# Kernel tuning notes

Measured on AMD Instinct MI355X. Metric: run time of the kernel, lower is better.

Reference implementation:

```python
import jax, jax.numpy as jnp
import numpy as np
import math

N_NODES = 100000
N_EDGES = 500000
HEADS = 8
IN_CH = 128          # dim(x) + dim(feats) = 64 + 64
OUT_CH = 128         # heads * 16
HEAD_DIM = OUT_CH // HEADS
MSG_DIM = 64
TIME_DIM = 64
EDGE_DIM = MSG_DIM + TIME_DIM


def setup_inputs() -> dict:
    key = jax.random.key(0)
    ks = jax.random.split(key, 16)
    p = lambda k, shp: (jax.random.normal(k, shp, dtype=jnp.float32) * 0.02)
    return {
        "feats": jax.random.normal(ks[0], (N_NODES, 64), dtype=jnp.float32),
        "x": jax.random.normal(ks[1], (N_NODES, 64), dtype=jnp.float32),
        "last_update": jax.random.uniform(ks[2], (N_NODES,), dtype=jnp.float32),
        "edge_index": jax.random.randint(ks[3], (2, N_EDGES), 0, N_NODES, dtype=jnp.int64),
        "t": jax.random.uniform(ks[4], (N_EDGES,), dtype=jnp.float32),
        "msg": jax.random.normal(ks[5], (N_EDGES, MSG_DIM), dtype=jnp.float32),
        # TimeEncoder: cos(Linear(1, TIME_DIM)(t))
        "time_w": p(ks[6], (TIME_DIM,)),
        "time_b": p(ks[7], (TIME_DIM,)),
        # TransformerConv params
        "Wq": p(ks[8], (IN_CH, OUT_CH)),
        "bq": jnp.zeros((OUT_CH,), jnp.float32),
        "Wk": p(ks[9], (IN_CH, OUT_CH)),
        "bk": jnp.zeros((OUT_CH,), jnp.float32),
        "Wv": p(ks[10], (IN_CH, OUT_CH)),
        "bv": jnp.zeros((OUT_CH,), jnp.float32),
        "We": p(ks[11], (EDGE_DIM, OUT_CH)),   # lin_edge, bias=False in PyG
        "Wskip": p(ks[12], (IN_CH, OUT_CH)),   # root weight skip connection
        "bskip": jnp.zeros((OUT_CH,), jnp.float32),
    }


def reference(feats, x, last_update, edge_index, t, msg,
              time_w, time_b, Wq, bq, Wk, bk, Wv, bv, We, Wskip, bskip):
    N = feats.shape[0]
    src, dst = edge_index[0], edge_index[1]  # message flows src -> dst

    # relative time encoding (TGN time encoder: cos(w*t + b))
    rel_t = last_update[src] - t                                  # [E]
    rel_t_enc = jnp.cos(rel_t[:, None] * time_w[None, :] + time_b)  # [E, TIME_DIM]
    edge_attr = jnp.concatenate([rel_t_enc, msg], axis=-1)        # [E, EDGE_DIM]

    h = jnp.concatenate([x, feats], axis=-1)                      # [N, IN_CH]

    q = (h @ Wq + bq).reshape(N, HEADS, HEAD_DIM)
    k = (h @ Wk + bk).reshape(N, HEADS, HEAD_DIM)
    v = (h @ Wv + bv).reshape(N, HEADS, HEAD_DIM)
    e = (edge_attr @ We).reshape(-1, HEADS, HEAD_DIM)             # [E, H, C]

    k_e = k[src] + e                                              # [E, H, C]
    alpha = jnp.sum(q[dst] * k_e, axis=-1) / math.sqrt(HEAD_DIM)  # [E, H]

    # segment softmax over incoming edges of each dst node
    m = jax.ops.segment_max(alpha, dst, num_segments=N)           # [N, H]
    m = jnp.where(jnp.isfinite(m), m, 0.0)
    ex = jnp.exp(alpha - m[dst])
    s = jax.ops.segment_sum(ex, dst, num_segments=N)              # [N, H]
    a = ex / (s[dst] + 1e-16)                                     # [E, H]

    out_e = (v[src] + e) * a[..., None]                           # [E, H, C]
    out = jax.ops.segment_sum(out_e, dst, num_segments=N)         # [N, H, C]
    out = out.reshape(N, HEADS * HEAD_DIM)
    return out + h @ Wskip + bskip
```

## Files before the change

kernel.cpp:

```cpp
#include <hip/hip_runtime.h>
#include <math.h>


typedef __attribute__((ext_vector_type(8))) short bf16x8;
typedef __attribute__((ext_vector_type(4))) float f32x4;

__device__ inline short f2bf(float f) {
  unsigned u = __float_as_uint(f);
  u += 0x7fff + ((u >> 16) & 1);
  return (short)(u >> 16);
}
__device__ inline float bf2f(short s) {
  return __uint_as_float(((unsigned)(unsigned short)s) << 16);
}
__device__ inline float bflo(unsigned u) { return __uint_as_float(u << 16); }
__device__ inline float bfhi(unsigned u) { return __uint_as_float(u & 0xffff0000u); }

__global__ void k_hist(const int* __restrict__ ei, int* __restrict__ counts, int E) {
  int i = blockIdx.x * 256 + threadIdx.x;
  if (i < E) atomicAdd(&counts[ei[E + i]], 1);
}

__global__ __launch_bounds__(1024) void k_bsum(const int* __restrict__ counts,
                                               int* __restrict__ bsum, int N) {
  int i = blockIdx.x * 1024 + threadIdx.x;
  int v = (i < N) ? counts[i] : 0;
  for (int d = 32; d; d >>= 1) v += __shfl_down(v, d);
  __shared__ int ws_[16];
  int lane = threadIdx.x & 63, wv = threadIdx.x >> 6;
  if (lane == 0) ws_[wv] = v;
  __syncthreads();
  if (threadIdx.x == 0) {
    int s = 0;
    for (int j = 0; j < 16; ++j) s += ws_[j];
    bsum[blockIdx.x] = s;
  }
}

__global__ __launch_bounds__(128) void k_bscan(const int* __restrict__ bsum,
                                               int* __restrict__ bpre, int nb) {
  __shared__ int sh[128];
  int t = threadIdx.x;
  sh[t] = (t < nb) ? bsum[t] : 0;
  __syncthreads();
  for (int d = 1; d < 128; d <<= 1) {
    int v = (t >= d) ? sh[t - d] : 0;
    __syncthreads();
    sh[t] += v;
    __syncthreads();
  }
  if (t < nb) bpre[t] = (t == 0) ? 0 : sh[t - 1];
}

__global__ __launch_bounds__(1024) void k_scan2(const int* __restrict__ counts,
                                                const int* __restrict__ bpre,
                                                int* __restrict__ offs,
                                                int* __restrict__ cursor, int N) {
  __shared__ int sh[1024];
  int t = threadIdx.x;
  int i = blockIdx.x * 1024 + t;
  int v = (i < N) ? counts[i] : 0;
  sh[t] = v;
  __syncthreads();
  for (int d = 1; d < 1024; d <<= 1) {
    int u = (t >= d) ? sh[t - d] : 0;
    __syncthreads();
    sh[t] += u;
    __syncthreads();
  }
  if (i < N) {
    int excl = bpre[blockIdx.x] + sh[t] - v;
    offs[i] = excl;
    cursor[i] = excl;
    if (i == N - 1) offs[N] = excl + v;
  }
}

__global__ void k_scatter(const int* __restrict__ ei, int* __restrict__ cursor,
                          int* __restrict__ rank, int* __restrict__ src_s, int E) {
  int i = blockIdx.x * 256 + threadIdx.x;
  if (i < E) {
    int pos = atomicAdd(&cursor[ei[E + i]], 1);
    rank[i] = pos;
    src_s[pos] = ei[i];
  }
}

struct PrepArgs { const float* W[5]; };
__global__ void k_prep(PrepArgs pa, short* __restrict__ wf) {
  int tid = blockIdx.x * 256 + threadIdx.x;
  if (tid >= 5 * 8 * 4 * 64) return;
  int lane = tid & 63;
  int kt = (tid >> 6) & 3;
  int nt = (tid >> 8) & 7;
  int mat = tid >> 11;
  const float* W = pa.W[mat];
  int n = nt * 16 + (lane & 15);
  short v[8];
#pragma unroll
  for (int j = 0; j < 8; ++j) {
    int k = kt * 32 + ((j >> 2) * 16) + ((lane >> 4) * 4) + (j & 3);
    v[j] = f2bf(W[k * 128 + n]);
  }
  ((uint4*)wf)[tid] = *(uint4*)v;
}

struct NodeArgs {
  const short* wf;
  const float* bias[4];
  void* outp[4];
};

__global__ __launch_bounds__(256, 2) void k_node(
    const float* __restrict__ x, const float* __restrict__ feats,
    NodeArgs na, int N) {
  __shared__ char lds[4][8192];
  const int lane = threadIdx.x & 63;
  const int wv = threadIdx.x >> 6;
  char* myl = lds[wv];

  bf16x8 bfrag[8][4];
  const uint4* wfp = (const uint4*)na.wf + (size_t)wv * 2048;
#pragma unroll
  for (int nt = 0; nt < 8; ++nt)
#pragma unroll
    for (int kt = 0; kt < 4; ++kt)
      *(uint4*)&bfrag[nt][kt] = wfp[(nt * 4 + kt) * 64 + lane];

  float biasv[8];
#pragma unroll
  for (int nt = 0; nt < 8; ++nt) biasv[nt] = na.bias[wv][nt * 16 + (lane & 15)];
  void* op = na.outp[wv];

  const int arow = lane & 15;
  const int k4 = (lane >> 4) * 4;
  const int ntiles = (N + 15) / 16;
  for (int tile = blockIdx.x; tile < ntiles; tile += gridDim.x) {
    int row = tile * 16 + arow;
    bool valid = row < N;
    const float* xr = x + (size_t)row * 64;
    const float* fr = feats + (size_t)row * 64;
    bf16x8 afrag[4];
#pragma unroll
    for (int kt = 0; kt < 4; ++kt) {
      const float* src = (kt < 2) ? xr : fr;
      int base = (kt & 1) * 32 + k4;
      float4 lo = valid ? *(const float4*)(src + base) : make_float4(0, 0, 0, 0);
      float4 hi = valid ? *(const float4*)(src + base + 16) : make_float4(0, 0, 0, 0);
      bf16x8 a;
      a[0] = f2bf(lo.x); a[1] = f2bf(lo.y); a[2] = f2bf(lo.z); a[3] = f2bf(lo.w);
      a[4] = f2bf(hi.x); a[5] = f2bf(hi.y); a[6] = f2bf(hi.z); a[7] = f2bf(hi.w);
      afrag[kt] = a;
    }
#pragma unroll
    for (int nt = 0; nt < 8; ++nt) {
      f32x4 acc = {0.f, 0.f, 0.f, 0.f};
#pragma unroll
      for (int kt = 0; kt < 4; ++kt)
        acc = __builtin_amdgcn_mfma_f32_16x16x32_bf16(afrag[kt], bfrag[nt][kt], acc, 0, 0, 0);
      int col = nt * 16 + (lane & 15);
#pragma unroll
      for (int reg = 0; reg < 4; ++reg) {
        int r = (lane >> 4) * 4 + reg;
        float vv = acc[reg] + biasv[nt];
        if (wv < 3) ((short*)myl)[r * 128 + col] = f2bf(vv);
        else        ((float*)myl)[r * 128 + col] = vv;
      }
    }
    if (wv < 3) {
      short* opp = (short*)op;
#pragma unroll
      for (int i = 0; i < 8; ++i) {
        int r = i * 2 + (lane >> 5);
        int orow = tile * 16 + r;
        uint2 val = ((const uint2*)myl)[i * 64 + lane];
        if (orow < N)
          *(uint2*)(opp + (size_t)orow * 128 + (lane & 31) * 4) = val;
      }
    } else {
      float* opp = (float*)op;
#pragma unroll
      for (int i = 0; i < 8; ++i) {
        int r = i * 2 + (lane >> 5);
        int orow = tile * 16 + r;
        uint4 val = ((const uint4*)myl)[i * 64 + lane];
        if (orow < N)
          *(uint4*)(opp + (size_t)orow * 128 + (lane & 31) * 4) = val;
      }
    }
  }
}

__global__ __launch_bounds__(512) void k_egemm(
    const float* __restrict__ lu, const int* __restrict__ ei,
    const float* __restrict__ t, const float* __restrict__ msg,
    const float* __restrict__ tw, const float* __restrict__ tb,
    const short* __restrict__ wf, const int* __restrict__ rank,
    short* __restrict__ e_s, int E) {
  __shared__ uint4 wlds[2048];
  __shared__ char tbuf[8][4096];
  const int lane = threadIdx.x & 63;
  const int wv = threadIdx.x >> 6;
  char* myl = tbuf[wv];

  for (int i = threadIdx.x; i < 2048; i += 512)
    wlds[i] = ((const uint4*)wf)[8192 + i];
  __syncthreads();

  const int k4 = (lane >> 4) * 4;
  float twv[16], tbv[16];
#pragma unroll
  for (int kt = 0; kt < 2; ++kt) {
    int base = kt * 32 + k4;
    *(float4*)&twv[kt * 8]     = *(const float4*)(tw + base);
    *(float4*)&twv[kt * 8 + 4] = *(const float4*)(tw + base + 16);
    *(float4*)&tbv[kt * 8]     = *(const float4*)(tb + base);
    *(float4*)&tbv[kt * 8 + 4] = *(const float4*)(tb + base + 16);
  }

  const int ntiles = (E + 15) / 16;
  const int nwaves = gridDim.x * 8;
  for (int tile = blockIdx.x * 8 + wv; tile < ntiles; tile += nwaves) {
    const int e0 = tile * 16;
    int rank16 = 0;
    float relt = 0.f;
    if (lane < 16 && e0 + lane < E) {
      int src = ei[e0 + lane];
      relt = lu[src] - t[e0 + lane];
      rank16 = rank[e0 + lane];
    }
    const int r = lane & 15;
    float my_relt = __shfl(relt, r);
    bool rvalid = (e0 + r) < E;

    bf16x8 afrag[4];
#pragma unroll
    for (int kt = 0; kt < 2; ++kt) {
      bf16x8 a;
#pragma unroll
      for (int j = 0; j < 8; ++j)
        a[j] = f2bf(__cosf(my_relt * twv[kt * 8 + j] + tbv[kt * 8 + j]));
      afrag[kt] = a;
    }
    const float* mr = msg + (size_t)(e0 + r) * 64;
#pragma unroll
    for (int kt = 2; kt < 4; ++kt) {
      int base = (kt - 2) * 32 + k4;
      float4 lo = rvalid ? *(const float4*)(mr + base) : make_float4(0, 0, 0, 0);
      float4 hi = rvalid ? *(const float4*)(mr + base + 16) : make_float4(0, 0, 0, 0);
      bf16x8 a;
      a[0] = f2bf(lo.x); a[1] = f2bf(lo.y); a[2] = f2bf(lo.z); a[3] = f2bf(lo.w);
      a[4] = f2bf(hi.x); a[5] = f2bf(hi.y); a[6] = f2bf(hi.z); a[7] = f2bf(hi.w);
      afrag[kt] = a;
    }

#pragma unroll
    for (int nt = 0; nt < 8; ++nt) {
      bf16x8 bfrag[4];
#pragma unroll
      for (int kt = 0; kt < 4; ++kt)
        *(uint4*)&bfrag[kt] = wlds[(nt * 4 + kt) * 64 + lane];
      f32x4 acc = {0.f, 0.f, 0.f, 0.f};
#pragma unroll
      for (int kt = 0; kt < 4; ++kt)
        acc = __builtin_amdgcn_mfma_f32_16x16x32_bf16(afrag[kt], bfrag[kt], acc, 0, 0, 0);
      int col = nt * 16 + (lane & 15);
#pragma unroll
      for (int reg = 0; reg < 4; ++reg) {
        int rr = (lane >> 4) * 4 + reg;
        ((short*)myl)[rr * 128 + col] = f2bf(acc[reg]);
      }
    }
#pragma unroll
    for (int i = 0; i < 8; ++i) {
      int rr = i * 2 + (lane >> 5);
      int er = e0 + rr;
      int drow = __shfl(rank16, rr);
      uint2 val = ((const uint2*)myl)[i * 64 + lane];
      if (er < E)
        *(uint2*)(e_s + (size_t)drow * 128 + (lane & 31) * 4) = val;
    }
  }
}

__global__ __launch_bounds__(256) void k_agg(
    const int* __restrict__ offs, const int* __restrict__ src_s,
    const short* __restrict__ e_s, const short* __restrict__ qb,
    const short* __restrict__ kb, const short* __restrict__ vb,
    float* __restrict__ out, int N) {
  __shared__ int lds_vo[4][64];
  const int wave = threadIdx.x >> 6;
  const int lane = threadIdx.x & 63;
  const int n = blockIdx.x * 4 + wave;
  if (n >= N) return;
  const int c2 = lane * 2;

  const int off = offs[n], end = offs[n + 1];
  unsigned qv = *(const unsigned*)(qb + (size_t)n * 128 + c2);
  float2 o = *(float2*)(out + (size_t)n * 128 + c2);
  if (end == off) return;
  const float q0 = bflo(qv), q1 = bfhi(qv);

  float s = 0.f, acc0 = 0.f, acc1 = 0.f;

  for (int c0 = off; c0 < end; c0 += 64) {
    const int cnt = min(64, end - c0);
    if (lane < cnt) lds_vo[wave][lane] = src_s[c0 + lane] * 128;
    const int lim = cnt - 1;
    for (int g0 = 0; g0 < cnt; g0 += 8) {
      unsigned evr[8], kvr[8], vvr[8];
#pragma unroll
      for (int g = 0; g < 8; ++g) {
        int jj = g0 + g;
        jj = (jj > lim) ? lim : jj;
        int vo = lds_vo[wave][jj];
        evr[g] = *(const unsigned*)(e_s + (size_t)(c0 + jj) * 128 + c2);
        kvr[g] = *(const unsigned*)(kb + vo + c2);
        vvr[g] = *(const unsigned*)(vb + vo + c2);
      }
#pragma unroll
      for (int g = 0; g < 8; ++g) {
        float part = q0 * (bflo(kvr[g]) + bflo(evr[g]))
                   + q1 * (bfhi(kvr[g]) + bfhi(evr[g]));
        part += __shfl_xor(part, 1);
        part += __shfl_xor(part, 2);
        part += __shfl_xor(part, 4);
        float p = (g0 + g <= lim) ? __expf(part * 0.25f) : 0.f;
        s += p;
        acc0 = fmaf(p, bflo(vvr[g]) + bflo(evr[g]), acc0);
        acc1 = fmaf(p, bfhi(vvr[g]) + bfhi(evr[g]), acc1);
      }
    }
  }
  float r = 1.f / (s + 1e-16f);
  o.x += acc0 * r;
  o.y += acc1 * r;
  *(float2*)(out + (size_t)n * 128 + c2) = o;
}

extern "C" void kernel_launch(void* const* d_in, const int* in_sizes, int n_in,
                              void* d_out, int out_size, void* d_ws, size_t ws_size,
                              hipStream_t stream) {
  const float* feats = (const float*)d_in[0];
  const float* x     = (const float*)d_in[1];
  const float* lu    = (const float*)d_in[2];
  const int*   ei    = (const int*)d_in[3];
  const float* t     = (const float*)d_in[4];
  const float* msg   = (const float*)d_in[5];
  const float* tw    = (const float*)d_in[6];
  const float* tb    = (const float*)d_in[7];
  const float* Wq    = (const float*)d_in[8];
  const float* bq    = (const float*)d_in[9];
  const float* Wk    = (const float*)d_in[10];
  const float* bk    = (const float*)d_in[11];
  const float* Wv    = (const float*)d_in[12];
  const float* bv    = (const float*)d_in[13];
  const float* We    = (const float*)d_in[14];
  const float* Wskip = (const float*)d_in[15];
  const float* bskip = (const float*)d_in[16];
  float* out = (float*)d_out;
  const int N = in_sizes[2];
  const int E = in_sizes[4];

  char* ws = (char*)d_ws;
  short* wfrag = (short*)ws; ws += 5 * 2048 * 16;
  short* qb    = (short*)ws; ws += (size_t)N * 128 * 2;
  short* kbuf  = (short*)ws; ws += (size_t)N * 128 * 2;
  short* vbuf  = (short*)ws; ws += (size_t)N * 128 * 2;
  short* e_s   = (short*)ws; ws += (size_t)E * 128 * 2;
  int* counts  = (int*)ws;   ws += (size_t)(N + 1) * 4;
  int* offs    = (int*)ws;   ws += (size_t)(N + 1) * 4;
  int* cursor  = (int*)ws;   ws += (size_t)N * 4;
  int* rank    = (int*)ws;   ws += (size_t)E * 4;
  int* src_s   = (int*)ws;   ws += (size_t)E * 4;
  int* bsum    = (int*)ws;   ws += 128 * 4;
  int* bpre    = (int*)ws;   ws += 128 * 4;

  const int nb = (N + 1023) / 1024;

  hipMemsetAsync(counts, 0, (size_t)(N + 1) * 4, stream);
  k_hist<<<(E + 255) / 256, 256, 0, stream>>>(ei, counts, E);
  k_bsum<<<nb, 1024, 0, stream>>>(counts, bsum, N);
  k_bscan<<<1, 128, 0, stream>>>(bsum, bpre, nb);
  k_scan2<<<nb, 1024, 0, stream>>>(counts, bpre, offs, cursor, N);
  k_scatter<<<(E + 255) / 256, 256, 0, stream>>>(ei, cursor, rank, src_s, E);

  PrepArgs pa;
  pa.W[0] = Wq; pa.W[1] = Wk; pa.W[2] = Wv; pa.W[3] = Wskip; pa.W[4] = We;
  k_prep<<<40, 256, 0, stream>>>(pa, wfrag);

  NodeArgs na;
  na.wf = wfrag;
  na.bias[0] = bq; na.bias[1] = bk; na.bias[2] = bv; na.bias[3] = bskip;
  na.outp[0] = qb; na.outp[1] = kbuf; na.outp[2] = vbuf; na.outp[3] = out;
  k_node<<<768, 256, 0, stream>>>(x, feats, na, N);

  k_egemm<<<512, 512, 0, stream>>>(lu, ei, t, msg, tw, tb, wfrag,
                                   rank, e_s, E);
  k_agg<<<(N + 3) / 4, 256, 0, stream>>>(offs, src_s, e_s, qb, kbuf, vbuf,
                                         out, N);
}
```

Before: 278.7 us.

## Process two nodes per wave in aggregation and swizzle LDS staging buffers

The aggregation kernel now assigns each half-wave to a separate destination node, with every lane handling four channels through 8-byte loads. This halves the number of idle lanes at low-degree nodes and cuts the shuffle reduction from three steps to two. Separately, the LDS staging buffers in the node and edge GEMMs use an XOR swizzle to reduce bank conflicts when writing the MFMA output. The cost is more registers per lane and less parallelism across channels for high-degree nodes.

```diff
diff --git a/kernel.cpp b/kernel.cpp
--- a/kernel.cpp
+++ b/kernel.cpp
@@ -163,8 +163,13 @@
       for (int reg = 0; reg < 4; ++reg) {
         int r = (lane >> 4) * 4 + reg;
         float vv = acc[reg] + biasv[nt];
-        if (wv < 3) ((short*)myl)[r * 128 + col] = f2bf(vv);
-        else        ((float*)myl)[r * 128 + col] = vv;
+        if (wv < 3) {
+          int wb = (r * 256 + col * 2) ^ (((r >> 2) & 3) << 5);
+          *(short*)(myl + wb) = f2bf(vv);
+        } else {
+          int wb = (r * 512 + col * 4) ^ (((r >> 2) & 3) << 6);
+          *(float*)(myl + wb) = vv;
+        }
       }
     }
     if (wv < 3) {
@@ -173,7 +178,8 @@
       for (int i = 0; i < 8; ++i) {
         int r = i * 2 + (lane >> 5);
         int orow = tile * 16 + r;
-        uint2 val = ((const uint2*)myl)[i * 64 + lane];
+        int rb = (r * 256 + (lane & 31) * 8) ^ (((r >> 2) & 3) << 5);
+        uint2 val = *(const uint2*)(myl + rb);
         if (orow < N)
           *(uint2*)(opp + (size_t)orow * 128 + (lane & 31) * 4) = val;
       }
@@ -183,7 +189,8 @@
       for (int i = 0; i < 8; ++i) {
         int r = i * 2 + (lane >> 5);
         int orow = tile * 16 + r;
-        uint4 val = ((const uint4*)myl)[i * 64 + lane];
+        int rb = (r * 512 + (lane & 31) * 16) ^ (((r >> 2) & 3) << 6);
+        uint4 val = *(const uint4*)(myl + rb);
         if (orow < N)
           *(uint4*)(opp + (size_t)orow * 128 + (lane & 31) * 4) = val;
       }
@@ -268,7 +275,8 @@
 #pragma unroll
       for (int reg = 0; reg < 4; ++reg) {
         int rr = (lane >> 4) * 4 + reg;
-        ((short*)myl)[rr * 128 + col] = f2bf(acc[reg]);
+        int wb = (rr * 256 + col * 2) ^ (((rr >> 2) & 3) << 5);
+        *(short*)(myl + wb) = f2bf(acc[reg]);
       }
     }
 #pragma unroll
@@ -276,7 +284,8 @@
       int rr = i * 2 + (lane >> 5);
       int er = e0 + rr;
       int drow = __shfl(rank16, rr);
-      uint2 val = ((const uint2*)myl)[i * 64 + lane];
+      int rb = (rr * 256 + (lane & 31) * 8) ^ (((rr >> 2) & 3) << 5);
+      uint2 val = *(const uint2*)(myl + rb);
       if (er < E)
         *(uint2*)(e_s + (size_t)drow * 128 + (lane & 31) * 4) = val;
     }
@@ -288,54 +297,61 @@
     const short* __restrict__ e_s, const short* __restrict__ qb,
     const short* __restrict__ kb, const short* __restrict__ vb,
     float* __restrict__ out, int N) {
-  __shared__ int lds_vo[4][64];
+  __shared__ int lds_vo[4][2][32];
   const int wave = threadIdx.x >> 6;
   const int lane = threadIdx.x & 63;
-  const int n = blockIdx.x * 4 + wave;
+  const int half = lane >> 5;
+  const int l32 = lane & 31;
+  const int n = blockIdx.x * 8 + wave * 2 + half;
   if (n >= N) return;
-  const int c2 = lane * 2;
+  const int c4 = l32 * 4;
 
   const int off = offs[n], end = offs[n + 1];
-  unsigned qv = *(const unsigned*)(qb + (size_t)n * 128 + c2);
-  float2 o = *(float2*)(out + (size_t)n * 128 + c2);
-  if (end == off) return;
-  const float q0 = bflo(qv), q1 = bfhi(qv);
-
-  float s = 0.f, acc0 = 0.f, acc1 = 0.f;
-
-  for (int c0 = off; c0 < end; c0 += 64) {
-    const int cnt = min(64, end - c0);
-    if (lane < cnt) lds_vo[wave][lane] = src_s[c0 + lane] * 128;
+  uint2 qv = *(const uint2*)(qb + (size_t)n * 128 + c4);
+  float4 o = *(float4*)(out + (size_t)n * 128 + c4);
+  const float q0 = bflo(qv.x), q1 = bfhi(qv.x);
+  const float q2 = bflo(qv.y), q3 = bfhi(qv.y);
+
+  float s = 0.f, a0 = 0.f, a1 = 0.f, a2 = 0.f, a3 = 0.f;
+
+  for (int c0 = off; c0 < end; c0 += 32) {
+    const int cnt = min(32, end - c0);
+    if (l32 < cnt) lds_vo[wave][half][l32] = src_s[c0 + l32] * 128;
     const int lim = cnt - 1;
     for (int g0 = 0; g0 < cnt; g0 += 8) {
-      unsigned evr[8], kvr[8], vvr[8];
+      uint2 evr[8], kvr[8], vvr[8];
 #pragma unroll
       for (int g = 0; g < 8; ++g) {
         int jj = g0 + g;
         jj = (jj > lim) ? lim : jj;
-        int vo = lds_vo[wave][jj];
-        evr[g] = *(const unsigned*)(e_s + (size_t)(c0 + jj) * 128 + c2);
-        kvr[g] = *(const unsigned*)(kb + vo + c2);
-        vvr[g] = *(const unsigned*)(vb + vo + c2);
+        int vo = lds_vo[wave][half][jj];
+        evr[g] = *(const uint2*)(e_s + (size_t)(c0 + jj) * 128 + c4);
+        kvr[g] = *(const uint2*)(kb + vo + c4);
+        vvr[g] = *(const uint2*)(vb + vo + c4);
       }
 #pragma unroll
       for (int g = 0; g < 8; ++g) {
-        float part = q0 * (bflo(kvr[g]) + bflo(evr[g]))
-                   + q1 * (bfhi(kvr[g]) + bfhi(evr[g]));
+        float part = q0 * (bflo(kvr[g].x) + bflo(evr[g].x))
+                   + q1 * (bfhi(kvr[g].x) + bfhi(evr[g].x))
+                   + q2 * (bflo(kvr[g].y) + bflo(evr[g].y))
+                   + q3 * (bfhi(kvr[g].y) + bfhi(evr[g].y));
         part += __shfl_xor(part, 1);
         part += __shfl_xor(part, 2);
-        part += __shfl_xor(part, 4);
         float p = (g0 + g <= lim) ? __expf(part * 0.25f) : 0.f;
         s += p;
-        acc0 = fmaf(p, bflo(vvr[g]) + bflo(evr[g]), acc0);
-        acc1 = fmaf(p, bfhi(vvr[g]) + bfhi(evr[g]), acc1);
+        a0 = fmaf(p, bflo(vvr[g].x) + bflo(evr[g].x), a0);
+        a1 = fmaf(p, bfhi(vvr[g].x) + bfhi(evr[g].x), a1);
+        a2 = fmaf(p, bflo(vvr[g].y) + bflo(evr[g].y), a2);
+        a3 = fmaf(p, bfhi(vvr[g].y) + bfhi(evr[g].y), a3);
       }
     }
   }
   float r = 1.f / (s + 1e-16f);
-  o.x += acc0 * r;
-  o.y += acc1 * r;
-  *(float2*)(out + (size_t)n * 128 + c2) = o;
+  o.x += a0 * r;
+  o.y += a1 * r;
+  o.z += a2 * r;
+  o.w += a3 * r;
+  *(float4*)(out + (size_t)n * 128 + c4) = o;
 }
 
 extern "C" void kernel_launch(void* const* d_in, const int* in_sizes, int n_in,
@@ -397,6 +413,6 @@
 
   k_egemm<<<512, 512, 0, stream>>>(lu, ei, t, msg, tw, tb, wfrag,
                                    rank, e_s, E);
-  k_agg<<<(N + 3) / 4, 256, 0, stream>>>(offs, src_s, e_s, qb, kbuf, vbuf,
+  k_agg<<<(N + 7) / 8, 256, 0, stream>>>(offs, src_s, e_s, qb, kbuf, vbuf,
                                          out, N);
 }
```

Measured after the change: 308.6 us. +10.7%, slower.

## Swizzle LDS staging tiles and process two destination nodes per wave

Applied to the files above, without the earlier changes.

Adds an XOR swizzle to the LDS staging buffers in the node and edge GEMM kernels, so the MFMA result scatter and the row readback avoid bank conflicts. The aggregation kernel now has each wave handle two consecutive destination nodes in sequence, halving the grid and sharing offset loads. Serialising the two nodes in one wave lowers parallelism and may hurt latency hiding for the gather-heavy aggregation.

```diff
diff --git a/kernel.cpp b/kernel.cpp
--- a/kernel.cpp
+++ b/kernel.cpp
@@ -163,8 +163,13 @@
       for (int reg = 0; reg < 4; ++reg) {
         int r = (lane >> 4) * 4 + reg;
         float vv = acc[reg] + biasv[nt];
-        if (wv < 3) ((short*)myl)[r * 128 + col] = f2bf(vv);
-        else        ((float*)myl)[r * 128 + col] = vv;
+        if (wv < 3) {
+          int wb = (r * 256 + col * 2) ^ (((r >> 2) & 3) << 5);
+          *(short*)(myl + wb) = f2bf(vv);
+        } else {
+          int wb = (r * 512 + col * 4) ^ (((r >> 2) & 3) << 6);
+          *(float*)(myl + wb) = vv;
+        }
       }
     }
     if (wv < 3) {
@@ -173,7 +178,8 @@
       for (int i = 0; i < 8; ++i) {
         int r = i * 2 + (lane >> 5);
         int orow = tile * 16 + r;
-        uint2 val = ((const uint2*)myl)[i * 64 + lane];
+        int rb = (r * 256 + (lane & 31) * 8) ^ (((r >> 2) & 3) << 5);
+        uint2 val = *(const uint2*)(myl + rb);
         if (orow < N)
           *(uint2*)(opp + (size_t)orow * 128 + (lane & 31) * 4) = val;
       }
@@ -183,7 +189,8 @@
       for (int i = 0; i < 8; ++i) {
         int r = i * 2 + (lane >> 5);
         int orow = tile * 16 + r;
-        uint4 val = ((const uint4*)myl)[i * 64 + lane];
+        int rb = (r * 512 + (lane & 31) * 16) ^ (((r >> 2) & 3) << 6);
+        uint4 val = *(const uint4*)(myl + rb);
         if (orow < N)
           *(uint4*)(opp + (size_t)orow * 128 + (lane & 31) * 4) = val;
       }
@@ -268,7 +275,8 @@
 #pragma unroll
       for (int reg = 0; reg < 4; ++reg) {
         int rr = (lane >> 4) * 4 + reg;
-        ((short*)myl)[rr * 128 + col] = f2bf(acc[reg]);
+        int wb = (rr * 256 + col * 2) ^ (((rr >> 2) & 3) << 5);
+        *(short*)(myl + wb) = f2bf(acc[reg]);
       }
     }
 #pragma unroll
@@ -276,7 +284,8 @@
       int rr = i * 2 + (lane >> 5);
       int er = e0 + rr;
       int drow = __shfl(rank16, rr);
-      uint2 val = ((const uint2*)myl)[i * 64 + lane];
+      int rb = (rr * 256 + (lane & 31) * 8) ^ (((rr >> 2) & 3) << 5);
+      uint2 val = *(const uint2*)(myl + rb);
       if (er < E)
         *(uint2*)(e_s + (size_t)drow * 128 + (lane & 31) * 4) = val;
     }
@@ -291,51 +300,65 @@
   __shared__ int lds_vo[4][64];
   const int wave = threadIdx.x >> 6;
   const int lane = threadIdx.x & 63;
-  const int n = blockIdx.x * 4 + wave;
-  if (n >= N) return;
+  const int n0 = (blockIdx.x * 4 + wave) * 2;
+  if (n0 >= N) return;
   const int c2 = lane * 2;
-
-  const int off = offs[n], end = offs[n + 1];
-  unsigned qv = *(const unsigned*)(qb + (size_t)n * 128 + c2);
-  float2 o = *(float2*)(out + (size_t)n * 128 + c2);
-  if (end == off) return;
-  const float q0 = bflo(qv), q1 = bfhi(qv);
-
-  float s = 0.f, acc0 = 0.f, acc1 = 0.f;
-
-  for (int c0 = off; c0 < end; c0 += 64) {
-    const int cnt = min(64, end - c0);
-    if (lane < cnt) lds_vo[wave][lane] = src_s[c0 + lane] * 128;
-    const int lim = cnt - 1;
-    for (int g0 = 0; g0 < cnt; g0 += 8) {
-      unsigned evr[8], kvr[8], vvr[8];
-#pragma unroll
-      for (int g = 0; g < 8; ++g) {
-        int jj = g0 + g;
-        jj = (jj > lim) ? lim : jj;
-        int vo = lds_vo[wave][jj];
-        evr[g] = *(const unsigned*)(e_s + (size_t)(c0 + jj) * 128 + c2);
-        kvr[g] = *(const unsigned*)(kb + vo + c2);
-        vvr[g] = *(const unsigned*)(vb + vo + c2);
+  const bool hasB = (n0 + 1) < N;
+
+  const int offA = offs[n0];
+  const int endA = offs[n0 + 1];
+  const int endB = hasB ? offs[n0 + 2] : endA;
+  const int offB = endA;
+  unsigned qvA = *(const unsigned*)(qb + (size_t)n0 * 128 + c2);
+  unsigned qvB = hasB ? *(const unsigned*)(qb + (size_t)(n0 + 1) * 128 + c2) : 0u;
+  float2 oA = *(float2*)(out + (size_t)n0 * 128 + c2);
+  float2 oB = hasB ? *(float2*)(out + (size_t)(n0 + 1) * 128 + c2)
+                   : make_float2(0.f, 0.f);
+
+  auto process = [&](int off, int end, unsigned qv, float2& o) {
+    if (end <= off) return;
+    const float q0 = bflo(qv), q1 = bfhi(qv);
+    float s = 0.f, acc0 = 0.f, acc1 = 0.f;
+    for (int c0 = off; c0 < end; c0 += 64) {
+      const int cnt = min(64, end - c0);
+      if (lane < cnt) lds_vo[wave][lane] = src_s[c0 + lane] * 128;
+      const int lim = cnt - 1;
+      for (int g0 = 0; g0 < cnt; g0 += 8) {
+        unsigned evr[8], kvr[8], vvr[8];
+#pragma unroll
+        for (int g = 0; g < 8; ++g) {
+          int jj = g0 + g;
+          jj = (jj > lim) ? lim : jj;
+          int vo = lds_vo[wave][jj];
+          evr[g] = *(const unsigned*)(e_s + (size_t)(c0 + jj) * 128 + c2);
+          kvr[g] = *(const unsigned*)(kb + vo + c2);
+          vvr[g] = *(const unsigned*)(vb + vo + c2);
+        }
+#pragma unroll
+        for (int g = 0; g < 8; ++g) {
+          float part = q0 * (bflo(kvr[g]) + bflo(evr[g]))
+                     + q1 * (bfhi(kvr[g]) + bfhi(evr[g]));
+          part += __shfl_xor(part, 1);
+          part += __shfl_xor(part, 2);
+          part += __shfl_xor(part, 4);
+          float p = (g0 + g <= lim) ? __expf(part * 0.25f) : 0.f;
+          s += p;
+          acc0 = fmaf(p, bflo(vvr[g]) + bflo(evr[g]), acc0);
+          acc1 = fmaf(p, bfhi(vvr[g]) + bfhi(evr[g]), acc1);
+        }
       }
-#pragma unroll
-      for (int g = 0; g < 8; ++g) {
-        float part = q0 * (bflo(kvr[g]) + bflo(evr[g]))
-                   + q1 * (bfhi(kvr[g]) + bfhi(evr[g]));
-        part += __shfl_xor(part, 1);
-        part += __shfl_xor(part, 2);
-        part += __shfl_xor(part, 4);
-        float p = (g0 + g <= lim) ? __expf(part * 0.25f) : 0.f;
-        s += p;
-        acc0 = fmaf(p, bflo(vvr[g]) + bflo(evr[g]), acc0);
-        acc1 = fmaf(p, bfhi(vvr[g]) + bfhi(evr[g]), acc1);
-      }
-    }
-  }
-  float r = 1.f / (s + 1e-16f);
-  o.x += acc0 * r;
-  o.y += acc1 * r;
-  *(float2*)(out + (size_t)n * 128 + c2) = o;
+    }
+    float r = 1.f / (s + 1e-16f);
+    o.x += acc0 * r;
+    o.y += acc1 * r;
+  };
+
+  process(offA, endA, qvA, oA);
+  *(float2*)(out + (size_t)n0 * 128 + c2) = oA;
+  if (hasB) {
+    process(offB, endB, qvB, oB);
+    *(float2*)(out + (size_t)(n0 + 1) * 128 + c2) = oB;
+  }
 }
 
 extern "C" void kernel_launch(void* const* d_in, const int* in_sizes, int n_in,
@@ -369,7 +392,7 @@
   short* vbuf  = (short*)ws; ws += (size_t)N * 128 * 2;
   short* e_s   = (short*)ws; ws += (size_t)E * 128 * 2;
   int* counts  = (int*)ws;   ws += (size_t)(N + 1) * 4;
-  int* offs    = (int*)ws;   ws += (size_t)(N + 1) * 4;
+  int* offs    = (int*)ws;   ws += (size_t)(N + 4) * 4;
   int* cursor  = (int*)ws;   ws += (size_t)N * 4;
   int* rank    = (int*)ws;   ws += (size_t)E * 4;
   int* src_s   = (int*)ws;   ws += (size_t)E * 4;
@@ -397,6 +420,6 @@
 
   k_egemm<<<512, 512, 0, stream>>>(lu, ei, t, msg, tw, tb, wfrag,
                                    rank, e_s, E);
-  k_agg<<<(N + 3) / 4, 256, 0, stream>>>(offs, src_s, e_s, qb, kbuf, vbuf,
+  k_agg<<<(N + 7) / 8, 256, 0, stream>>>(offs, src_s, e_s, qb, kbuf, vbuf,
                                          out, N);
 }
```

After: 280.6 us. About the same (+0.7%).
